# Kernel optimization log

Measured on AMD Instinct MI355X. Metric: run time of the kernel, lower is better.

The kernel has to match this reference:

```python
import jax, jax.numpy as jnp
import numpy as np

RPN_BATCH = 256
ROI_BATCH = 128
IMG = 800.0


def _box_iou(a, b):
    # a: [N,4], b: [G,4] -> [N,G]
    lt = jnp.maximum(a[:, None, :2], b[None, :, :2])
    rb = jnp.minimum(a[:, None, 2:], b[None, :, 2:])
    wh = jnp.clip(rb - lt, 0.0)
    inter = wh[..., 0] * wh[..., 1]
    area_a = (a[:, 2] - a[:, 0]) * (a[:, 3] - a[:, 1])
    area_b = (b[:, 2] - b[:, 0]) * (b[:, 3] - b[:, 1])
    return inter / (area_a[:, None] + area_b[None, :] - inter + 1e-6)


def _encode(a, t):
    wa = a[:, 2] - a[:, 0]
    ha = a[:, 3] - a[:, 1]
    xa = a[:, 0] + 0.5 * wa
    ya = a[:, 1] + 0.5 * ha
    wt = t[:, 2] - t[:, 0]
    ht = t[:, 3] - t[:, 1]
    xt = t[:, 0] + 0.5 * wt
    yt = t[:, 1] + 0.5 * ht
    return jnp.stack(((xt - xa) / wa, (yt - ya) / ha,
                      jnp.log(wt / wa + 1e-6), jnp.log(ht / ha + 1e-6)), axis=1)


def _smooth_l1(x):
    ax = jnp.abs(x)
    return jnp.where(ax < 1.0, 0.5 * x * x, ax - 0.5)


def _rpn_loss_one(scores, deltas, anchors, gt):
    # scores [N,1], deltas [N,4], anchors [N,4], gt [G,4]
    ious = _box_iou(anchors, gt)                 # [N,G]
    max_iou = ious.max(axis=1)
    argmax = ious.argmax(axis=1)
    labels = jnp.full((anchors.shape[0],), -1.0, dtype=scores.dtype)
    labels = jnp.where(max_iou < 0.3, 0.0, labels)
    labels = jnp.where(max_iou > 0.7, 1.0, labels)
    labels = labels.at[jnp.argmax(ious, axis=0)].set(1.0)  # each gt's best anchor is positive
    # deterministic subsampling: keep first K in index order (replaces randperm)
    num_pos = RPN_BATCH // 2
    pos = labels == 1.0
    labels = jnp.where(pos & (jnp.cumsum(pos) > num_pos), -1.0, labels)
    n_pos = jnp.sum(labels == 1.0)
    neg = labels == 0.0
    labels = jnp.where(neg & (jnp.cumsum(neg) > (RPN_BATCH - n_pos)), -1.0, labels)
    mask = (labels != -1.0).astype(scores.dtype)
    logit = scores[:, 0]
    t = jnp.clip(labels, 0.0, 1.0)
    bce = jnp.maximum(logit, 0.0) - logit * t + jnp.log1p(jnp.exp(-jnp.abs(logit)))
    cls = jnp.sum(bce * mask) / jnp.maximum(jnp.sum(mask), 1.0)
    tgt = _encode(anchors, gt[argmax])
    posm = (labels == 1.0).astype(scores.dtype)
    n_posf = jnp.sum(posm)
    reg = jnp.where(n_posf > 0,
                    jnp.sum(_smooth_l1(deltas - tgt) * posm[:, None])
                    / jnp.maximum(n_posf * 4.0, 1.0),
                    0.0)
    return cls + reg


def _det_loss_one(cls_scores, bbox_deltas, proposals, gt, gt_labels):
    # cls_scores [P,C], bbox_deltas [P,4C], proposals [P,4], gt [G,4], gt_labels [G]
    P = proposals.shape[0]
    ious = _box_iou(proposals, gt)
    max_iou = ious.max(axis=1)
    argmax = ious.argmax(axis=1)
    assigned = jnp.where(max_iou >= 0.5, gt_labels[argmax], 0)
    num_pos = ROI_BATCH // 4
    pos = assigned > 0
    pos_rank = jnp.cumsum(pos) - 1
    neg_rank = jnp.cumsum(~pos) - 1
    idx = jnp.arange(P)
    # sort key: first up-to-num_pos positives (index order), then negatives,
    # excess positives pushed to the end -> first ROI_BATCH entries are the sample
    key = jnp.where(pos,
                    jnp.where(pos_rank < num_pos, pos_rank, 2 * P + idx),
                    P + neg_rank)
    sampled = jnp.argsort(key)[:ROI_BATCH]
    t_labels = assigned[sampled]
    matched = gt[argmax[sampled]]
    t_deltas = _encode(proposals[sampled], matched)
    logp = jax.nn.log_softmax(cls_scores[sampled], axis=-1)
    cls = -jnp.mean(jnp.take_along_axis(logp, t_labels[:, None], axis=1)[:, 0])
    pd = bbox_deltas[sampled].reshape(ROI_BATCH, -1, 4)
    preds = pd[jnp.arange(ROI_BATCH), t_labels]  # class-specific deltas
    posm = (t_labels > 0).astype(cls_scores.dtype)
    n_pos = jnp.sum(posm)
    reg = jnp.where(n_pos > 0,
                    jnp.sum(_smooth_l1(preds - t_deltas) * posm[:, None])
                    / jnp.maximum(n_pos * 4.0, 1.0),
                    0.0)
    return cls + reg


def _rand_boxes(k, prefix):
    k1, k2 = jax.random.split(k)
    xy = jax.random.uniform(k1, prefix + (2,)) * (IMG - 130.0)
    wh = jax.random.uniform(k2, prefix + (2,)) * 120.0 + 8.0
    return jnp.concatenate([xy, xy + wh], axis=-1)


def setup_inputs() -> dict:
    B, N, P, G, C = 4, 250000, 1000, 32, 81
    key = jax.random.key(0)
    ks = jax.random.split(key, 8)
    return {
        "rpn_scores": jax.random.normal(ks[0], (B, N, 1), dtype=jnp.float32),
        "rpn_deltas": jax.random.normal(ks[1], (B, N, 4), dtype=jnp.float32) * 0.1,
        "cls_scores": jax.random.normal(ks[2], (B * P, C), dtype=jnp.float32),
        "bbox_deltas": jax.random.normal(ks[3], (B * P, 4 * C), dtype=jnp.float32) * 0.1,
        "anchors": _rand_boxes(ks[4], (N,)),
        "proposals": _rand_boxes(ks[5], (B, P)),
        "gt_boxes": _rand_boxes(ks[6], (B, G)),
        "gt_labels": jax.random.randint(ks[7], (B, G), 1, C, dtype=jnp.int32),
    }


def reference(rpn_scores, rpn_deltas, cls_scores, bbox_deltas,
              anchors, proposals, gt_boxes, gt_labels):
    B, P, _ = proposals.shape
    C = cls_scores.shape[-1]
    cls_b = cls_scores.reshape(B, P, C)
    del_b = bbox_deltas.reshape(B, P, 4 * C)
    rpn = jax.vmap(lambda s, d, g: _rpn_loss_one(s, d, anchors, g))(
        rpn_scores, rpn_deltas, gt_boxes)
    det = jax.vmap(_det_loss_one)(cls_b, del_b, proposals, gt_boxes, gt_labels)
    return jnp.sum(rpn) + jnp.sum(det)
```

## Files before the change

kernel.cpp:

```cpp
#include <hip/hip_runtime.h>
#include <math.h>
#include <stdint.h>

#define B_ 4
#define N_ 250000
#define P_ 1000
#define G_ 32
#define C_ 81
#define RPN_BATCH 256
#define ROI_BATCH 128

#define ABLK 1024
#define NBA ((N_ + ABLK - 1) / ABLK)
#define DETB 4

__device__ __forceinline__ float iou_one(float a0, float a1, float a2, float a3,
                                         float areaA,
                                         float b0, float b1, float b2, float b3) {
    float ltx = fmaxf(a0, b0), lty = fmaxf(a1, b1);
    float rbx = fminf(a2, b2), rby = fminf(a3, b3);
    float w = fmaxf(rbx - ltx, 0.f), h = fmaxf(rby - lty, 0.f);
    float inter = w * h;
    float areaB = (b2 - b0) * (b3 - b1);
    return inter / (areaA + areaB - inter + 1e-6f);
}

__device__ __forceinline__ float smooth_l1(float x) {
    float ax = fabsf(x);
    return (ax < 1.f) ? 0.5f * x * x : ax - 0.5f;
}

__global__ void __launch_bounds__(256, 4) rpn_assign_det(
        const float* __restrict__ anchors, const float* __restrict__ gt_boxes,
        const int* __restrict__ gt_labels, const float* __restrict__ proposals,
        const float* __restrict__ cls_scores, const float* __restrict__ bbox_deltas,
        int8_t* __restrict__ labels, int* __restrict__ posCnt, int* __restrict__ negCnt,
        unsigned long long* __restrict__ gtWin, float* __restrict__ detPart,
        float* __restrict__ out, int out_size) {
    int b = blockIdx.y, tid = threadIdx.x;
    int lane = tid & 63, wave = tid >> 6;

    if (blockIdx.x >= NBA) {
        int h = blockIdx.x - NBA;
        __shared__ float sgt[G_ * 4];
        __shared__ int sgl[G_];
        __shared__ short sassign[P_];
        __shared__ unsigned char sargm[P_];
        __shared__ int ssamp[ROI_BATCH];
        __shared__ int swd[4];
        __shared__ float sc[4], srg[4];
        if (tid < G_ * 4) sgt[tid] = gt_boxes[b * G_ * 4 + tid];
        if (tid < G_) sgl[tid] = gt_labels[b * G_ + tid];
        __syncthreads();

        int myPos = 0;
        int labj[4];
#pragma unroll
        for (int j = 0; j < 4; ++j) {
            int p = tid * 4 + j;
            int labp = 0, am = 0;
            if (p < P_) {
                float4 A = ((const float4*)proposals)[b * P_ + p];
                float areaA = (A.z - A.x) * (A.w - A.y);
                float best = -1.f;
#pragma unroll 8
                for (int g = 0; g < G_; ++g) {
                    float iou = iou_one(A.x, A.y, A.z, A.w, areaA,
                                        sgt[g * 4], sgt[g * 4 + 1], sgt[g * 4 + 2], sgt[g * 4 + 3]);
                    if (iou > best) { best = iou; am = g; }
                }
                labp = (best >= 0.5f) ? sgl[am] : 0;
                sassign[p] = (short)labp;
                sargm[p] = (unsigned char)am;
                labj[j] = labp;
                myPos += (labp > 0);
            } else {
                labj[j] = -1;
            }
        }

        int inc = myPos;
        for (int off = 1; off < 64; off <<= 1) {
            int v = __shfl_up(inc, off);
            if (lane >= off) inc += v;
        }
        if (lane == 63) swd[wave] = inc;
        __syncthreads();
        int basew = 0, total = 0;
        for (int w = 0; w < 4; ++w) { if (w < wave) basew += swd[w]; total += swd[w]; }
        int pp = basew + inc - myPos;
        int npos_kept = min(total, ROI_BATCH / 4);
        int nneg_total = P_ - total;
#pragma unroll
        for (int j = 0; j < 4; ++j) {
            int p = tid * 4 + j;
            if (labj[j] < 0) break;
            int slot;
            if (labj[j] > 0) {
                slot = (pp < ROI_BATCH / 4) ? pp : npos_kept + nneg_total + (pp - ROI_BATCH / 4);
                pp++;
            } else {
                slot = npos_kept + (p - pp);
            }
            if (slot < ROI_BATCH) ssamp[slot] = p;
        }
        int np_det = npos_kept + max(0, ROI_BATCH - npos_kept - nneg_total);
        __syncthreads();

        int rowBase = h * (ROI_BATCH / DETB) + wave * 8;
        float clsAcc = 0.f;
        for (int k = 0; k < 8; k += 2) {
            int s0 = ssamp[rowBase + k], s1 = ssamp[rowBase + k + 1];
            const float* r0 = cls_scores + ((size_t)(b * P_ + s0)) * C_;
            const float* r1 = cls_scores + ((size_t)(b * P_ + s1)) * C_;
            float a1 = r0[lane], b1 = r1[lane];
            float a2 = (lane < C_ - 64) ? r0[64 + lane] : -INFINITY;
            float b2 = (lane < C_ - 64) ? r1[64 + lane] : -INFINITY;
            float m0 = fmaxf(a1, a2), m1 = fmaxf(b1, b2);
            for (int mm = 32; mm >= 1; mm >>= 1) {
                m0 = fmaxf(m0, __shfl_xor(m0, mm));
                m1 = fmaxf(m1, __shfl_xor(m1, mm));
            }
            float e0 = expf(a1 - m0) + ((lane < C_ - 64) ? expf(a2 - m0) : 0.f);
            float e1 = expf(b1 - m1) + ((lane < C_ - 64) ? expf(b2 - m1) : 0.f);
            for (int mm = 32; mm >= 1; mm >>= 1) {
                e0 += __shfl_xor(e0, mm);
                e1 += __shfl_xor(e1, mm);
            }
            int t0 = sassign[s0], t1 = sassign[s1];
            int q0 = (t0 < 64) ? t0 : t0 - 64;
            int q1 = (t1 < 64) ? t1 : t1 - 64;
            float lo0 = __shfl(a1, q0), hi0 = __shfl(a2, q0);
            float lo1 = __shfl(b1, q1), hi1 = __shfl(b2, q1);
            float v0 = (t0 < 64) ? lo0 : hi0;
            float v1 = (t1 < 64) ? lo1 : hi1;
            if (lane == 0)
                clsAcc += -(v0 - m0 - logf(e0)) - (v1 - m1 - logf(e1));
        }

        float regAcc = 0.f;
        if (lane < 8) {
            int r = rowBase + lane;
            int s = ssamp[r];
            int t = sassign[s];
            if (t > 0) {
                int g = sargm[s];
                float4 A = ((const float4*)proposals)[b * P_ + s];
                float t0g = sgt[g * 4], t1g = sgt[g * 4 + 1];
                float t2g = sgt[g * 4 + 2], t3g = sgt[g * 4 + 3];
                float wa = A.z - A.x, ha = A.w - A.y;
                float xa = A.x + 0.5f * wa, ya = A.y + 0.5f * ha;
                float wt = t2g - t0g, ht = t3g - t1g;
                float xt = t0g + 0.5f * wt, yt = t1g + 0.5f * ht;
                const float4 pd = *(const float4*)(bbox_deltas +
                        ((size_t)(b * P_ + s)) * (4 * C_) + 4 * t);
                regAcc = smooth_l1(pd.x - (xt - xa) / wa) + smooth_l1(pd.y - (yt - ya) / ha) +
                         smooth_l1(pd.z - logf(wt / wa + 1e-6f)) +
                         smooth_l1(pd.w - logf(ht / ha + 1e-6f));
            }
        }
        for (int mm = 32; mm >= 1; mm >>= 1) regAcc += __shfl_xor(regAcc, mm);
        if (lane == 0) { sc[wave] = clsAcc; srg[wave] = regAcc; }
        __syncthreads();
        if (tid == 0) {
            float cp = sc[0] + sc[1] + sc[2] + sc[3];
            float rp = srg[0] + srg[1] + srg[2] + srg[3];
            detPart[b * DETB + h] = cp / (float)ROI_BATCH +
                ((np_det > 0) ? rp / fmaxf((float)np_det * 4.f, 1.f) : 0.f);
        }
        return;
    }

    __shared__ float4 sA[ABLK];
    __shared__ unsigned char sPart[4][ABLK];
    __shared__ int sCnt[8];

    int base = blockIdx.x * ABLK;

    if (blockIdx.x == 0 && b == 0) {
        for (int i = tid; i < out_size; i += 256) out[i] = 0.f;
    }

    for (int t = tid; t < ABLK; t += 256) {
        int ai = base + t;
        float4 v = make_float4(0.f, 0.f, 0.f, 0.f);
        if (ai < N_) v = ((const float4*)anchors)[ai];
        sA[t] = v;
    }
    __syncthreads();

    int waveu = __builtin_amdgcn_readfirstlane(wave);

    const float4* gt4 = (const float4*)gt_boxes + b * G_ + waveu * 8;
    float g0[8], g1[8], g2[8], g3[8], gae[8];
#pragma unroll
    for (int j = 0; j < 8; ++j) {
        float4 g = gt4[j];
        g0[j] = g.x; g1[j] = g.y; g2[j] = g.z; g3[j] = g.w;
        gae[j] = (g.z - g.x) * (g.w - g.y) + 1e-6f;
    }

    float bi[8], bd[8]; int bx[8];
#pragma unroll
    for (int j = 0; j < 8; ++j) { bi[j] = 0.f; bd[j] = 1.f; bx[j] = 0; }

    for (int k = 0; k < ABLK / 64; ++k) {
        int a = k * 64 + lane;
        float4 A = sA[a];
        float areaA = (A.z - A.x) * (A.w - A.y);
        int gidx = base + a;
        float acc03 = 1e30f, acc07 = 1e30f;
#pragma unroll
        for (int j = 0; j < 8; ++j) {
            float ltx = fmaxf(A.x, g0[j]), lty = fmaxf(A.y, g1[j]);
            float rbx = fminf(A.z, g2[j]), rby = fminf(A.w, g3[j]);
            float w = fmaxf(rbx - ltx, 0.f), h = fmaxf(rby - lty, 0.f);
            float inter = w * h;
            float d = (areaA + gae[j]) - inter;
            acc03 = fminf(acc03, fmaf(0.3f, d, -inter));
            acc07 = fminf(acc07, fmaf(0.7f, d, -inter));
            float p1 = inter * bd[j], p2 = bi[j] * d;
            if (p1 > p2) { bi[j] = inter; bd[j] = d; bx[j] = gidx; }
        }
        sPart[wave][a] = (unsigned char)(((acc07 < 0.f) ? 2 : 0) | ((acc03 > 0.f) ? 1 : 0));
    }

#pragma unroll
    for (int j = 0; j < 8; ++j) {
        float i_ = bi[j], d_ = bd[j]; int x_ = bx[j];
        for (int m = 32; m >= 1; m >>= 1) {
            float oi = __shfl_xor(i_, m), od = __shfl_xor(d_, m);
            int ox = __shfl_xor(x_, m);
            float pa = oi * d_, pb = i_ * od;
            bool take = (pa > pb) || (pa == pb && ox < x_);
            if (take) { i_ = oi; d_ = od; x_ = ox; }
        }
        if (lane == 0) {
            float iou = i_ / d_;
            unsigned long long pk =
                (((unsigned long long)__float_as_uint(iou)) << 32) |
                (unsigned)(0xFFFFFFFFu - (unsigned)x_);
            atomicMax(&gtWin[(size_t)b * G_ + wave * 8 + j], pk);
        }
    }
    __syncthreads();

    unsigned u0 = ((const unsigned*)&sPart[0][0])[tid];
    unsigned u1 = ((const unsigned*)&sPart[1][0])[tid];
    unsigned u2 = ((const unsigned*)&sPart[2][0])[tid];
    unsigned u3 = ((const unsigned*)&sPart[3][0])[tid];
    unsigned andb = u0 & u1 & u2 & u3;
    unsigned orb  = u0 | u1 | u2 | u3;
    int gbase = base + tid * 4;
    unsigned outw = 0; int cp = 0, cn = 0;
#pragma unroll
    for (int j = 0; j < 4; ++j) {
        int above = (orb >> (8 * j + 1)) & 1;
        int below = (andb >> (8 * j)) & 1;
        int lab = above ? 1 : (below ? 0 : -1);
        if (gbase + j < N_) { cp += (lab == 1); cn += (lab == 0); }
        outw |= ((unsigned)(unsigned char)(char)lab) << (8 * j);
    }
    if (gbase < N_)
        ((unsigned*)labels)[(((size_t)b * N_ + base) >> 2) + tid] = outw;

    for (int m = 32; m >= 1; m >>= 1) { cp += __shfl_xor(cp, m); cn += __shfl_xor(cn, m); }
    if (lane == 0) { sCnt[wave] = cp; sCnt[4 + wave] = cn; }
    __syncthreads();
    if (tid == 0) {
        posCnt[b * NBA + blockIdx.x] = sCnt[0] + sCnt[1] + sCnt[2] + sCnt[3];
        negCnt[b * NBA + blockIdx.x] = sCnt[4] + sCnt[5] + sCnt[6] + sCnt[7];
    }
}

__global__ void __launch_bounds__(256) rpn_sample(
        const int8_t* __restrict__ labels, const float* __restrict__ rpn_scores,
        const float* __restrict__ rpn_deltas, const float* __restrict__ anchors,
        const float* __restrict__ gt_boxes,
        const int* __restrict__ posCnt, const int* __restrict__ negCnt,
        const unsigned long long* __restrict__ gtWin,
        const float* __restrict__ detPart, float* __restrict__ out) {
    int b = blockIdx.y, tid = threadIdx.x;
    int base = blockIdx.x * ABLK;
    __shared__ float sg[G_ * 4];
    __shared__ int sp[256], sn[256];
    __shared__ unsigned swin[G_];
    __shared__ int sBase[6];
    __shared__ int swP[4], swN[4];
    __shared__ float sred[8];

    if (tid < G_ * 4) sg[tid] = gt_boxes[b * G_ * 4 + tid];
    if (tid < G_) {
        unsigned long long v = gtWin[(size_t)b * G_ + tid];
        swin[tid] = 0xFFFFFFFFu - (unsigned)(v & 0xFFFFFFFFull);
    }
    sp[tid] = (tid < NBA) ? posCnt[b * NBA + tid] : 0;
    sn[tid] = (tid < NBA) ? negCnt[b * NBA + tid] : 0;
    __syncthreads();

    if (tid < G_) {
        unsigned w = swin[tid];
        bool first = true;
        for (int j = 0; j < tid; ++j) if (swin[j] == w) first = false;
        if (first) {
            int8_t old = labels[(size_t)b * N_ + w];
            int blk = (int)(w / ABLK);
            if (old != 1) atomicAdd(&sp[blk], 1);
            if (old == 0) atomicAdd(&sn[blk], -1);
        }
    }
    __syncthreads();

    int vp = sp[tid], vn = sn[tid];
    for (int off = 1; off < 256; off <<= 1) {
        int tp = 0, tn = 0;
        if (tid >= off) { tp = sp[tid - off]; tn = sn[tid - off]; }
        __syncthreads();
        sp[tid] += tp; sn[tid] += tn;
        __syncthreads();
    }
    if (tid == blockIdx.x) {
        sBase[0] = sp[tid] - vp; sBase[1] = sn[tid] - vn;
        sBase[4] = vp; sBase[5] = vn;
    }
    if (tid == 255) { sBase[2] = sp[255]; sBase[3] = sn[255]; }
    __syncthreads();

    int posB = sBase[0], negB = sBase[1], totP = sBase[2], totN = sBase[3];
    int cPblk = sBase[4], cNblk = sBase[5];
    int npos = min(totP, RPN_BATCH / 2);
    int negQ = RPN_BATCH - npos;
    bool active = (cPblk > 0 && posB < RPN_BATCH / 2) || (cNblk > 0 && negB < negQ);
    if (!active && blockIdx.x != 0) return;

    int gbase = base + tid * 4;
    unsigned word = 0xFFFFFFFFu;
    if (gbase < N_)
        word = ((const unsigned*)labels)[(((size_t)b * N_ + base) >> 2) + tid];
    int lab[4];
#pragma unroll
    for (int j = 0; j < 4; ++j) lab[j] = (int)(char)((word >> (8 * j)) & 0xFF);
    for (int g = 0; g < G_; ++g) {
        int d = (int)swin[g] - gbase;
        if (d >= 0 && d < 4) lab[d] = 1;
    }
    int cntP = 0, cntN = 0;
#pragma unroll
    for (int j = 0; j < 4; ++j) {
        if (gbase + j < N_) { cntP += (lab[j] == 1); cntN += (lab[j] == 0); }
    }

    int lane = tid & 63, wave = tid >> 6;
    int ip = cntP, inn = cntN;
    for (int off = 1; off < 64; off <<= 1) {
        int vpp = __shfl_up(ip, off), vnn = __shfl_up(inn, off);
        if (lane >= off) { ip += vpp; inn += vnn; }
    }
    if (lane == 63) { swP[wave] = ip; swN[wave] = inn; }
    __syncthreads();
    int bP = 0, bN = 0;
    for (int w = 0; w < wave; ++w) { bP += swP[w]; bN += swN[w]; }
    int pP = posB + bP + ip - cntP;
    int pN = negB + bN + inn - cntN;

    float bce = 0.f, regv = 0.f;
#pragma unroll
    for (int j = 0; j < 4; ++j) {
        int i = gbase + j;
        if (i >= N_) break;
        if (lab[j] == 1) {
            int r = pP++;
            if (r < RPN_BATCH / 2) {
                float l = rpn_scores[(size_t)b * N_ + i];
                bce += fmaxf(l, 0.f) - l + log1pf(expf(-fabsf(l)));
                float4 A = ((const float4*)anchors)[i];
                float areaA = (A.z - A.x) * (A.w - A.y);
                float best = -1.f; int am = 0;
                for (int g = 0; g < G_; ++g) {
                    float iou = iou_one(A.x, A.y, A.z, A.w, areaA,
                                        sg[g * 4], sg[g * 4 + 1], sg[g * 4 + 2], sg[g * 4 + 3]);
                    if (iou > best) { best = iou; am = g; }
                }
                float t0 = sg[am * 4], t1 = sg[am * 4 + 1], t2 = sg[am * 4 + 2], t3 = sg[am * 4 + 3];
                float wa = A.z - A.x, ha = A.w - A.y;
                float xa = A.x + 0.5f * wa, ya = A.y + 0.5f * ha;
                float wt = t2 - t0, ht = t3 - t1;
                float xt = t0 + 0.5f * wt, yt = t1 + 0.5f * ht;
                float4 D = ((const float4*)rpn_deltas)[(size_t)b * N_ + i];
                regv += smooth_l1(D.x - (xt - xa) / wa) + smooth_l1(D.y - (yt - ya) / ha) +
                        smooth_l1(D.z - logf(wt / wa + 1e-6f)) + smooth_l1(D.w - logf(ht / ha + 1e-6f));
            }
        } else if (lab[j] == 0) {
            int r = pN++;
            if (r < negQ) {
                float l = rpn_scores[(size_t)b * N_ + i];
                bce += fmaxf(l, 0.f) + log1pf(expf(-fabsf(l)));
            }
        }
    }
    for (int m = 32; m >= 1; m >>= 1) { bce += __shfl_xor(bce, m); regv += __shfl_xor(regv, m); }
    if (lane == 0) { sred[wave] = bce; sred[4 + wave] = regv; }
    __syncthreads();
    if (tid == 0) {
        float sb = sred[0] + sred[1] + sred[2] + sred[3];
        float sr = sred[4] + sred[5] + sred[6] + sred[7];
        int rnp = min(totP, RPN_BATCH / 2);
        int kneg = min(totN, RPN_BATCH - rnp);
        float denomC = fmaxf((float)(rnp + kneg), 1.f);
        float contrib = sb / denomC +
                        ((rnp > 0) ? sr / fmaxf((float)rnp * 4.f, 1.f) : 0.f);
        if (blockIdx.x == 0)
            contrib += detPart[b * DETB + 0] + detPart[b * DETB + 1] +
                       detPart[b * DETB + 2] + detPart[b * DETB + 3];
        if (contrib != 0.f || blockIdx.x == 0) atomicAdd(out, contrib);
    }
}

extern "C" void kernel_launch(void* const* d_in, const int* in_sizes, int n_in,
                              void* d_out, int out_size, void* d_ws, size_t ws_size,
                              hipStream_t stream) {
    const float* rpn_scores  = (const float*)d_in[0];
    const float* rpn_deltas  = (const float*)d_in[1];
    const float* cls_scores  = (const float*)d_in[2];
    const float* bbox_deltas = (const float*)d_in[3];
    const float* anchors     = (const float*)d_in[4];
    const float* proposals   = (const float*)d_in[5];
    const float* gt_boxes    = (const float*)d_in[6];
    const int*   gt_labels   = (const int*)d_in[7];
    float* out = (float*)d_out;

    char* ws = (char*)d_ws;
    size_t off = 0;
    auto alloc = [&](size_t bytes) -> char* {
        size_t o = (off + 255) & ~(size_t)255;
        off = o + bytes;
        return ws + o;
    };
    int8_t* labels = (int8_t*)alloc((size_t)B_ * N_);
    int* posCnt = (int*)alloc((size_t)B_ * NBA * 4);
    int* negCnt = (int*)alloc((size_t)B_ * NBA * 4);
    unsigned long long* gtWin = (unsigned long long*)alloc(B_ * G_ * 8);
    float* detPart = (float*)alloc(B_ * DETB * 4);

    hipMemsetAsync(gtWin, 0, B_ * G_ * 8, stream);
    rpn_assign_det<<<dim3(NBA + DETB, B_), 256, 0, stream>>>(
            anchors, gt_boxes, gt_labels, proposals, cls_scores, bbox_deltas,
            labels, posCnt, negCnt, gtWin, detPart, out, out_size);
    rpn_sample<<<dim3(NBA, B_), 256, 0, stream>>>(labels, rpn_scores, rpn_deltas,
                                                  anchors, gt_boxes, posCnt, negCnt,
                                                  gtWin, detPart, out);
}
```

Measured before the change: 164.6 us.

## Replace global atomicMax gt-winner with per-block partials and wave-scan block prefix

Each assign block now writes its per-gt best packed IoU/index to a per-block slot instead of issuing a 64-bit atomicMax on a shared global word. Every sample block then reduces all block partials itself using shuffles, which also removes the memset launch. The block-count prefix sum moves from a shared-memory Hillis-Steele scan with many barriers to a wave shuffle scan plus a cross-wave combine. The trade-off is that the reduction is repeated redundantly in every sample block (about 32x245 loads each), in exchange for no atomic contention and one fewer launch.

Result: faster. 141.5 us (-14.0%).

```diff
diff --git a/kernel.cpp b/kernel.cpp
--- a/kernel.cpp
+++ b/kernel.cpp
@@ -25,6 +25,13 @@
     return inter / (areaA + areaB - inter + 1e-6f);
 }
 
+__device__ __forceinline__ unsigned long long shfl_xor_u64(unsigned long long v, int m) {
+    unsigned lo = (unsigned)v, hi = (unsigned)(v >> 32);
+    lo = __shfl_xor(lo, m);
+    hi = __shfl_xor(hi, m);
+    return ((unsigned long long)hi << 32) | lo;
+}
+
 __device__ __forceinline__ float smooth_l1(float x) {
     float ax = fabsf(x);
     return (ax < 1.f) ? 0.5f * x * x : ax - 0.5f;
@@ -35,7 +42,7 @@
         const int* __restrict__ gt_labels, const float* __restrict__ proposals,
         const float* __restrict__ cls_scores, const float* __restrict__ bbox_deltas,
         int8_t* __restrict__ labels, int* __restrict__ posCnt, int* __restrict__ negCnt,
-        unsigned long long* __restrict__ gtWin, float* __restrict__ detPart,
+        unsigned long long* __restrict__ blockBest, float* __restrict__ detPart,
         float* __restrict__ out, int out_size) {
     int b = blockIdx.y, tid = threadIdx.x;
     int lane = tid & 63, wave = tid >> 6;
@@ -240,7 +247,7 @@
             unsigned long long pk =
                 (((unsigned long long)__float_as_uint(iou)) << 32) |
                 (unsigned)(0xFFFFFFFFu - (unsigned)x_);
-            atomicMax(&gtWin[(size_t)b * G_ + wave * 8 + j], pk);
+            blockBest[((size_t)b * G_ + wave * 8 + j) * NBA + blockIdx.x] = pk;
         }
     }
     __syncthreads();
@@ -278,24 +285,36 @@
         const float* __restrict__ rpn_deltas, const float* __restrict__ anchors,
         const float* __restrict__ gt_boxes,
         const int* __restrict__ posCnt, const int* __restrict__ negCnt,
-        const unsigned long long* __restrict__ gtWin,
+        const unsigned long long* __restrict__ blockBest,
         const float* __restrict__ detPart, float* __restrict__ out) {
     int b = blockIdx.y, tid = threadIdx.x;
     int base = blockIdx.x * ABLK;
+    int lane = tid & 63, wave = tid >> 6;
     __shared__ float sg[G_ * 4];
     __shared__ int sp[256], sn[256];
     __shared__ unsigned swin[G_];
     __shared__ int sBase[6];
+    __shared__ int sWT[8];
     __shared__ int swP[4], swN[4];
     __shared__ float sred[8];
 
     if (tid < G_ * 4) sg[tid] = gt_boxes[b * G_ * 4 + tid];
-    if (tid < G_) {
-        unsigned long long v = gtWin[(size_t)b * G_ + tid];
-        swin[tid] = 0xFFFFFFFFu - (unsigned)(v & 0xFFFFFFFFull);
-    }
     sp[tid] = (tid < NBA) ? posCnt[b * NBA + tid] : 0;
     sn[tid] = (tid < NBA) ? negCnt[b * NBA + tid] : 0;
+
+    {
+        int g = tid >> 3, sub = tid & 7;
+        unsigned long long v = 0;
+        for (int j = sub; j < NBA; j += 8) {
+            unsigned long long x = blockBest[((size_t)b * G_ + g) * NBA + j];
+            if (x > v) v = x;
+        }
+        for (int m = 4; m >= 1; m >>= 1) {
+            unsigned long long o = shfl_xor_u64(v, m);
+            if (o > v) v = o;
+        }
+        if (sub == 0) swin[g] = 0xFFFFFFFFu - (unsigned)(v & 0xFFFFFFFFull);
+    }
     __syncthreads();
 
     if (tid < G_) {
@@ -312,18 +331,21 @@
     __syncthreads();
 
     int vp = sp[tid], vn = sn[tid];
-    for (int off = 1; off < 256; off <<= 1) {
-        int tp = 0, tn = 0;
-        if (tid >= off) { tp = sp[tid - off]; tn = sn[tid - off]; }
-        __syncthreads();
-        sp[tid] += tp; sn[tid] += tn;
-        __syncthreads();
-    }
+    int ipp = vp, inn2 = vn;
+    for (int off = 1; off < 64; off <<= 1) {
+        int a = __shfl_up(ipp, off), c = __shfl_up(inn2, off);
+        if (lane >= off) { ipp += a; inn2 += c; }
+    }
+    if (lane == 63) { sWT[wave] = ipp; sWT[4 + wave] = inn2; }
+    __syncthreads();
+    int preP = 0, preN = 0;
+    for (int w = 0; w < wave; ++w) { preP += sWT[w]; preN += sWT[4 + w]; }
+    int inclP = preP + ipp, inclN = preN + inn2;
     if (tid == blockIdx.x) {
-        sBase[0] = sp[tid] - vp; sBase[1] = sn[tid] - vn;
+        sBase[0] = inclP - vp; sBase[1] = inclN - vn;
         sBase[4] = vp; sBase[5] = vn;
     }
-    if (tid == 255) { sBase[2] = sp[255]; sBase[3] = sn[255]; }
+    if (tid == 255) { sBase[2] = inclP; sBase[3] = inclN; }
     __syncthreads();
 
     int posB = sBase[0], negB = sBase[1], totP = sBase[2], totN = sBase[3];
@@ -350,7 +372,6 @@
         if (gbase + j < N_) { cntP += (lab[j] == 1); cntN += (lab[j] == 0); }
     }
 
-    int lane = tid & 63, wave = tid >> 6;
     int ip = cntP, inn = cntN;
     for (int off = 1; off < 64; off <<= 1) {
         int vpp = __shfl_up(ip, off), vnn = __shfl_up(inn, off);
@@ -439,14 +460,13 @@
     int8_t* labels = (int8_t*)alloc((size_t)B_ * N_);
     int* posCnt = (int*)alloc((size_t)B_ * NBA * 4);
     int* negCnt = (int*)alloc((size_t)B_ * NBA * 4);
-    unsigned long long* gtWin = (unsigned long long*)alloc(B_ * G_ * 8);
+    unsigned long long* blockBest = (unsigned long long*)alloc((size_t)B_ * G_ * NBA * 8);
     float* detPart = (float*)alloc(B_ * DETB * 4);
 
-    hipMemsetAsync(gtWin, 0, B_ * G_ * 8, stream);
     rpn_assign_det<<<dim3(NBA + DETB, B_), 256, 0, stream>>>(
             anchors, gt_boxes, gt_labels, proposals, cls_scores, bbox_deltas,
-            labels, posCnt, negCnt, gtWin, detPart, out, out_size);
+            labels, posCnt, negCnt, blockBest, detPart, out, out_size);
     rpn_sample<<<dim3(NBA, B_), 256, 0, stream>>>(labels, rpn_scores, rpn_deltas,
                                                   anchors, gt_boxes, posCnt, negCnt,
-                                                  gtWin, detPart, out);
-}
+                                                  blockBest, detPart, out);
+}
```
